# Kernel optimization log

Measured on AMD Instinct MI355X. Metric: run time of the kernel, lower is better.

## Reference

```python
import jax, jax.numpy as jnp
import numpy as np

B, T, D = 8, 1024, 1024
H, HS = 16, 64  # num_heads, head_size; H*HS == D


def setup_inputs() -> dict:
    key = jax.random.key(0)
    ks = jax.random.split(key, 5)
    scale = 0.02
    x = jax.random.normal(ks[0], (B, T, D), dtype=jnp.float32)
    Wq = jax.random.normal(ks[1], (H, D, HS), dtype=jnp.float32) * scale
    Wk = jax.random.normal(ks[2], (H, D, HS), dtype=jnp.float32) * scale
    Wv = jax.random.normal(ks[3], (H, D, HS), dtype=jnp.float32) * scale
    Wo = jax.random.normal(ks[4], (D, D), dtype=jnp.float32) * scale
    bo = jnp.zeros((D,), dtype=jnp.float32)
    return {"x": x, "Wq": Wq, "Wk": Wk, "Wv": Wv, "Wo": Wo, "bo": bo}


def reference(x, Wq, Wk, Wv, Wo, bo):
    # Per-head linear projections (bias-free, as in Head): [B,H,T,HS]
    q = jnp.einsum('btd,hds->bhts', x, Wq)
    k = jnp.einsum('btd,hds->bhts', x, Wk)
    v = jnp.einsum('btd,hds->bhts', x, Wv)
    # Scaled scores with causal mask: [B,H,T,T]
    scores = jnp.einsum('bhts,bhus->bhtu', q, k) * (HS ** -0.5)
    causal = jnp.tril(jnp.ones((T, T), dtype=bool))
    scores = jnp.where(causal, scores, jnp.finfo(scores.dtype).min)
    att = jax.nn.softmax(scores, axis=-1)
    # Weighted sum over values, then concat heads: [B,T,H*HS]
    out = jnp.einsum('bhtu,bhus->bhts', att, v)
    out = out.transpose(0, 2, 1, 3).reshape(B, T, H * HS)
    # Output projection (nn.Linear: y = x @ W^T + b)
    return out @ Wo.T + bo
```

## Files before the change

### kernel.cpp

```cpp
#include <hip/hip_runtime.h>
#include <hip/hip_bf16.h>

#define BBATCH 8
#define TSEQ   1024
#define DMODEL 1024
#define NHEAD  16
#define HSZ    64

typedef unsigned short ushort_t;
typedef __attribute__((ext_vector_type(8))) short short8;
typedef __attribute__((ext_vector_type(4))) float float4v;

__device__ __forceinline__ ushort_t f2bf(float f) {
    __hip_bfloat16 h = __float2bfloat16(f);
    return *reinterpret_cast<ushort_t*>(&h);
}
__device__ __forceinline__ ushort_t f2bf_fast(float f) {
    return (ushort_t)((__float_as_uint(f) + 0x8000u) >> 16);
}
__device__ __forceinline__ unsigned int pack_bf2(float lo, float hi) {
    unsigned int a = __float_as_uint(lo) + 0x8000u;
    unsigned int b = __float_as_uint(hi) + 0x8000u;
    return __builtin_amdgcn_perm(b, a, 0x07060302u);
}

__device__ __forceinline__ short8 cvt8(const float* f) {
    union { ushort_t u[8]; short8 v; } r;
    #pragma unroll
    for (int e = 0; e < 8; ++e) r.u[e] = f2bf(f[e]);
    return r.v;
}

__device__ __forceinline__ void async16(const ushort_t* g, ushort_t* l) {
    __builtin_amdgcn_global_load_lds(
        (const __attribute__((address_space(1))) unsigned int*)g,
        (__attribute__((address_space(3))) unsigned int*)l, 16, 0, 0);
}

template<int N> __device__ __forceinline__ void vwait() {
    if constexpr (N == 3)      asm volatile("s_waitcnt vmcnt(3)" ::: "memory");
    else if constexpr (N == 0) asm volatile("s_waitcnt vmcnt(0)" ::: "memory");
}

__global__ __launch_bounds__(256) void cvt_f32_bf16(
    const float* __restrict__ src, ushort_t* __restrict__ dst)
{
    const size_t idx = ((size_t)blockIdx.x * 256 + threadIdx.x) * 16;
    float f[16];
    *(float4*)(f + 0)  = *(const float4*)(src + idx);
    *(float4*)(f + 4)  = *(const float4*)(src + idx + 4);
    *(float4*)(f + 8)  = *(const float4*)(src + idx + 8);
    *(float4*)(f + 12) = *(const float4*)(src + idx + 12);
    uint4 o0 = make_uint4(pack_bf2(f[0], f[1]),   pack_bf2(f[2], f[3]),
                          pack_bf2(f[4], f[5]),   pack_bf2(f[6], f[7]));
    uint4 o1 = make_uint4(pack_bf2(f[8], f[9]),   pack_bf2(f[10], f[11]),
                          pack_bf2(f[12], f[13]), pack_bf2(f[14], f[15]));
    *(uint4*)(dst + idx) = o0;
    *(uint4*)(dst + idx + 8) = o1;
}

__global__ __launch_bounds__(256) void pack_w(
    const float* __restrict__ Wq, const float* __restrict__ Wk,
    const float* __restrict__ Wv, ushort_t* __restrict__ WpT)
{
    __shared__ ushort_t L[64 * 72];
    const int tid = threadIdx.x;
    const int d0 = blockIdx.x * 64;
    const int wh = blockIdx.y;
    const int w = wh >> 4, h = wh & 15;
    const float* W = (w == 0 ? Wq : (w == 1 ? Wk : Wv)) + (size_t)h * DMODEL * HSZ;

    int dr = tid >> 2, sc = (tid & 3) * 16;
    const float4* src = (const float4*)(W + (size_t)(d0 + dr) * HSZ + sc);
    float f[16];
    *(float4*)(f + 0) = src[0]; *(float4*)(f + 4) = src[1];
    *(float4*)(f + 8) = src[2]; *(float4*)(f + 12) = src[3];
    *(short8*)(L + dr * 72 + sc)     = cvt8(f);
    *(short8*)(L + dr * 72 + sc + 8) = cvt8(f + 8);
    __syncthreads();

    int s = tid >> 2, dc = (tid & 3) * 16;
    union { ushort_t u[16]; short8 v[2]; } o;
    #pragma unroll
    for (int j = 0; j < 16; ++j) o.u[j] = L[(dc + j) * 72 + s];
    ushort_t* dst = WpT + (size_t)(w * 1024 + h * 64 + s) * DMODEL + d0 + dc;
    *(short8*)dst = o.v[0];
    *(short8*)(dst + 8) = o.v[1];
}

template<bool STG, int VW>
__device__ __forceinline__ void kstep32(
    const ushort_t* Ab, const ushort_t* Bb,
    ushort_t* An, ushort_t* Bn,
    const ushort_t*& gA, const ushort_t*& gB,
    const int wave,
    const int (&aoff)[4], const int (&boff)[4],
    float4v (&acc)[4][4])
{
    short8 av[4], bv[4];
    #pragma unroll
    for (int a = 0; a < 4; ++a) av[a] = *(const short8*)(Ab + aoff[a]);
    #pragma unroll
    for (int b = 0; b < 4; ++b) bv[b] = *(const short8*)(Bb + boff[b]);
    if (STG) {
        async16(gA,                An + wave * 512);
        async16(gB,                Bn + wave * 512);
        async16(gB + 128 * DMODEL, Bn + 4096 + wave * 512);
        gA += 32; gB += 32;
    }
    __builtin_amdgcn_s_setprio(1);
    #pragma unroll
    for (int a = 0; a < 4; ++a)
        #pragma unroll
        for (int b = 0; b < 4; ++b)
            acc[a][b] = __builtin_amdgcn_mfma_f32_16x16x32_bf16(
                av[a], bv[b], acc[a][b], 0, 0, 0);
    __builtin_amdgcn_s_setprio(0);
    vwait<VW>();
    __builtin_amdgcn_s_barrier();
}

__global__ __launch_bounds__(512, 4) void qkv_gemm(
    const ushort_t* __restrict__ Xb, const ushort_t* __restrict__ WpT,
    ushort_t* __restrict__ Qb, ushort_t* __restrict__ Kb, ushort_t* __restrict__ Vt)
{
    __shared__ ushort_t Ab[3][128 * 32];
    __shared__ ushort_t Bb[3][256 * 32];

    const int tid = threadIdx.x;
    const int wave = tid >> 6, lane = tid & 63;
    const int q = lane >> 4, cc = lane & 15;
    const int wm = wave >> 2, wn = wave & 3;

    const int bid = blockIdx.x;
    const int xcd = bid & 7;
    const bool isV = (bid >= 512);
    int ta, tb;
    if (!isV) {
        int lo = bid >> 3;
        ta = lo >> 2;
        tb = xcd * 4 + (lo & 3);
    } else {
        int lo = (bid - 512) >> 3;
        ta = xcd * 8 + (lo & 7);
        tb = lo >> 3;
    }
    const ushort_t* pA = isV ? Xb  + (size_t)ta * 128 * DMODEL
                             : WpT + (size_t)ta * 128 * DMODEL;
    const ushort_t* pB = isV ? WpT + (size_t)(2048 + tb * 256) * DMODEL
                             : Xb  + (size_t)tb * 256 * DMODEL;

    const int srow = lane >> 2;
    const int chx = (lane & 3) ^ ((lane >> 3) & 3);
    const ushort_t* gA = pA + (size_t)(wave * 16 + srow) * DMODEL + chx * 8;
    const ushort_t* gB = pB + (size_t)(wave * 16 + srow) * DMODEL + chx * 8;

    int aoff[4], boff[4];
    const int cswz = (q ^ ((cc >> 1) & 3)) * 8;
    #pragma unroll
    for (int f = 0; f < 4; ++f) {
        aoff[f] = (wm * 64 + f * 16 + cc) * 32 + cswz;
        boff[f] = (wn * 64 + f * 16 + cc) * 32 + cswz;
    }

    float4v acc[4][4];
    #pragma unroll
    for (int a = 0; a < 4; ++a)
        #pragma unroll
        for (int b = 0; b < 4; ++b) acc[a][b] = (float4v){0.f, 0.f, 0.f, 0.f};

    async16(gA,                Ab[0] + wave * 512);
    async16(gB,                Bb[0] + wave * 512);
    async16(gB + 128 * DMODEL, Bb[0] + 4096 + wave * 512);
    gA += 32; gB += 32;
    async16(gA,                Ab[1] + wave * 512);
    async16(gB,                Bb[1] + wave * 512);
    async16(gB + 128 * DMODEL, Bb[1] + 4096 + wave * 512);
    gA += 32; gB += 32;
    vwait<3>();
    __builtin_amdgcn_s_barrier();

    #pragma unroll 1
    for (int it = 0; it < 10; ++it) {
        kstep32<true, 3>(Ab[0], Bb[0], Ab[2], Bb[2], gA, gB, wave, aoff, boff, acc);
        kstep32<true, 3>(Ab[1], Bb[1], Ab[0], Bb[0], gA, gB, wave, aoff, boff, acc);
        kstep32<true, 3>(Ab[2], Bb[2], Ab[1], Bb[1], gA, gB, wave, aoff, boff, acc);
    }
    kstep32<false, 0>(Ab[0], Bb[0], Ab[2], Bb[2], gA, gB, wave, aoff, boff, acc);
    kstep32<false, -1>(Ab[1], Bb[1], Ab[0], Bb[0], gA, gB, wave, aoff, boff, acc);

    if (!isV) {
        ushort_t* Out = (ta < 8) ? Qb : Kb;
        const float osc = (ta < 8) ? 0.18033688011112042f : 1.0f;
        const int h = ((ta * 128 + wm * 64) >> 6) & 15;
        #pragma unroll
        for (int b = 0; b < 4; ++b) {
            int mc = tb * 256 + wn * 64 + b * 16 + cc;
            int bb = mc >> 10, t = mc & 1023;
            size_t rb = (((size_t)(bb * NHEAD + h)) * TSEQ + t) * HSZ;
            #pragma unroll
            for (int a = 0; a < 4; ++a) {
                int s0 = a * 16 + q * 4;
                uint2 pk = make_uint2(
                    pack_bf2(acc[a][b][0] * osc, acc[a][b][1] * osc),
                    pack_bf2(acc[a][b][2] * osc, acc[a][b][3] * osc));
                *(uint2*)(Out + rb + s0) = pk;
            }
        }
    } else {
        #pragma unroll
        for (int b = 0; b < 4; ++b) {
            int nc = tb * 256 + wn * 64 + b * 16 + cc;
            int h = nc >> 6, s = nc & 63;
            #pragma unroll
            for (int a = 0; a < 4; ++a) {
                int mr = ta * 128 + wm * 64 + a * 16 + q * 4;
                int bb = mr >> 10, t0 = mr & 1023;
                size_t addr = (((size_t)(bb * NHEAD + h)) * HSZ + s) * TSEQ + t0;
                uint2 pk = make_uint2(pack_bf2(acc[a][b][0], acc[a][b][1]),
                                      pack_bf2(acc[a][b][2], acc[a][b][3]));
                *(uint2*)(Vt + addr) = pk;
            }
        }
    }
}

__global__ __launch_bounds__(256) void attn(
    const ushort_t* __restrict__ Qb, const ushort_t* __restrict__ Kb,
    const ushort_t* __restrict__ Vt, ushort_t* __restrict__ Ob)
{
    __shared__ ushort_t Ks[2][64 * 64];
    __shared__ ushort_t VTs[2][64 * 64];
    __shared__ ushort_t Ps[4][32 * 72];
    const int tid = threadIdx.x;
    const int wave = tid >> 6, lane = tid & 63;
    const int q = lane >> 4, cc = lane & 15;
    const int bid = blockIdx.x;
    const int qt = 7 - (bid >> 7);
    const int bh = bid & 127;
    const size_t base = (size_t)bh * TSEQ * HSZ;
    const int J = 2 * qt + 2;

    const ushort_t* kg[2]; const ushort_t* vg[2]; int dmo[2];
    #pragma unroll
    for (int i = 0; i < 2; ++i) {
        int rr = wave * 16 + i * 8 + (lane >> 3);
        int ch = (lane & 7) ^ (rr & 7);
        kg[i] = Kb + base + (size_t)rr * HSZ + ch * 8;
        vg[i] = Vt + base + (size_t)rr * TSEQ + ch * 8;
        dmo[i] = (wave * 16 + i * 8) * 64;
    }

    short8 qf[2][2];
    #pragma unroll
    for (int tt = 0; tt < 2; ++tt) {
        const ushort_t* qp = Qb + base +
            (size_t)(qt * 128 + wave * 32 + tt * 16 + cc) * HSZ + q * 8;
        qf[tt][0] = *(const short8*)qp;
        qf[tt][1] = *(const short8*)(qp + 32);
    }

    int koff[4][2], poff[2][2];
    #pragma unroll
    for (int ut = 0; ut < 4; ++ut)
        #pragma unroll
        for (int kt = 0; kt < 2; ++kt)
            koff[ut][kt] = (ut * 16 + cc) * 64 + (((kt * 4 + q) ^ (cc & 7)) * 8);
    #pragma unroll
    for (int tt = 0; tt < 2; ++tt)
        #pragma unroll
        for (int kt = 0; kt < 2; ++kt)
            poff[tt][kt] = (tt * 16 + cc) * 72 + kt * 32 + q * 8;

    float4v oacc[2][4];
    #pragma unroll
    for (int tt = 0; tt < 2; ++tt)
        #pragma unroll
        for (int st = 0; st < 4; ++st) oacc[tt][st] = (float4v){0.f, 0.f, 0.f, 0.f};
    float lsum[2] = {0.f, 0.f};

    #pragma unroll
    for (int i = 0; i < 2; ++i) {
        async16(kg[i], &Ks[0][dmo[i]]);
        async16(vg[i], &VTs[0][dmo[i]]);
    }
    __syncthreads();

    for (int jt = 0; jt < J; ++jt) {
        const ushort_t* Kc = Ks[jt & 1];
        const ushort_t* Vc = VTs[jt & 1];
        if (jt + 1 < J) {
            int nb = (jt + 1) & 1;
            #pragma unroll
            for (int i = 0; i < 2; ++i) {
                async16(kg[i] + (size_t)(jt + 1) * 64 * HSZ, &Ks[nb][dmo[i]]);
                async16(vg[i] + (jt + 1) * 64, &VTs[nb][dmo[i]]);
            }
        }

        float4v sc[4][2];
        #pragma unroll
        for (int ut = 0; ut < 4; ++ut)
            #pragma unroll
            for (int tt = 0; tt < 2; ++tt) sc[ut][tt] = (float4v){0.f, 0.f, 0.f, 0.f};
        #pragma unroll
        for (int kt = 0; kt < 2; ++kt) {
            short8 kf[4];
            #pragma unroll
            for (int ut = 0; ut < 4; ++ut) kf[ut] = *(const short8*)(Kc + koff[ut][kt]);
            #pragma unroll
            for (int ut = 0; ut < 4; ++ut) {
                sc[ut][0] = __builtin_amdgcn_mfma_f32_16x16x32_bf16(
                    kf[ut], qf[0][kt], sc[ut][0], 0, 0, 0);
                sc[ut][1] = __builtin_amdgcn_mfma_f32_16x16x32_bf16(
                    kf[ut], qf[1][kt], sc[ut][1], 0, 0, 0);
            }
        }

        if ((jt >> 1) == qt) {
            #pragma unroll
            for (int tt = 0; tt < 2; ++tt) {
                const int tg = qt * 128 + wave * 32 + tt * 16 + cc;
                #pragma unroll
                for (int ut = 0; ut < 4; ++ut) {
                    float pv[4]; float ps = 0.f;
                    #pragma unroll
                    for (int rr = 0; rr < 4; ++rr) {
                        float p = exp2f(sc[ut][tt][rr]);
                        if ((jt * 64 + ut * 16 + q * 4 + rr) > tg) p = 0.f;
                        pv[rr] = p; ps += p;
                    }
                    lsum[tt] += ps;
                    *(uint2*)&Ps[wave][(tt * 16 + cc) * 72 + ut * 16 + q * 4] =
                        make_uint2(pack_bf2(pv[0], pv[1]), pack_bf2(pv[2], pv[3]));
                }
            }
        } else {
            #pragma unroll
            for (int tt = 0; tt < 2; ++tt) {
                #pragma unroll
                for (int ut = 0; ut < 4; ++ut) {
                    float pv[4]; float ps = 0.f;
                    #pragma unroll
                    for (int rr = 0; rr < 4; ++rr) {
                        float p = exp2f(sc[ut][tt][rr]);
                        pv[rr] = p; ps += p;
                    }
                    lsum[tt] += ps;
                    *(uint2*)&Ps[wave][(tt * 16 + cc) * 72 + ut * 16 + q * 4] =
                        make_uint2(pack_bf2(pv[0], pv[1]), pack_bf2(pv[2], pv[3]));
                }
            }
        }

        #pragma unroll
        for (int kt = 0; kt < 2; ++kt) {
            short8 pa0 = *(const short8*)&Ps[wave][poff[0][kt]];
            short8 pa1 = *(const short8*)&Ps[wave][poff[1][kt]];
            #pragma unroll
            for (int st = 0; st < 4; ++st) {
                short8 vf = *(const short8*)(Vc + koff[st][kt]);
                oacc[0][st] = __builtin_amdgcn_mfma_f32_16x16x32_bf16(
                    pa0, vf, oacc[0][st], 0, 0, 0);
                oacc[1][st] = __builtin_amdgcn_mfma_f32_16x16x32_bf16(
                    pa1, vf, oacc[1][st], 0, 0, 0);
            }
        }
        __syncthreads();
    }

    float inv[2];
    #pragma unroll
    for (int tt = 0; tt < 2; ++tt) {
        float l = lsum[tt];
        l += __shfl_xor(l, 16);
        l += __shfl_xor(l, 32);
        inv[tt] = 1.f / l;
    }
    const int b = bh >> 4, h = bh & 15;
    #pragma unroll
    for (int tt = 0; tt < 2; ++tt)
        #pragma unroll
        for (int rr = 0; rr < 4; ++rr) {
            float iv = __shfl(inv[tt], q * 4 + rr);
            int t = qt * 128 + wave * 32 + tt * 16 + q * 4 + rr;
            size_t rb = ((size_t)b * TSEQ + t) * DMODEL + h * HSZ;
            #pragma unroll
            for (int st = 0; st < 4; ++st)
                Ob[rb + st * 16 + cc] = f2bf_fast(oacc[tt][st][rr] * iv);
        }
}

__global__ __launch_bounds__(256) void oproj_gemm(
    const ushort_t* __restrict__ Obuf, const ushort_t* __restrict__ Wob,
    const float* __restrict__ bo, float* __restrict__ out)
{
    __shared__ ushort_t As[128 * 64];
    __shared__ ushort_t Bs[128 * 64];
    const int tid = threadIdx.x;
    const int wave = tid >> 6, lane = tid & 63;
    const int q = lane >> 4, cc = lane & 15;
    const int bid = blockIdx.x;
    const int xcd = bid & 7, local = bid >> 3;
    const int n0 = (local >> 3) * 128;
    const int m0 = (xcd * 8 + (local & 7)) * 128;
    const int wm = wave >> 1, wn = wave & 1;

    const ushort_t* ag[4]; const ushort_t* bg[4]; int lo_[4];
    #pragma unroll
    for (int i = 0; i < 4; ++i) {
        int row = wave * 32 + i * 8 + (lane >> 3);
        int ch = (lane & 7) ^ (row & 7);
        ag[i] = Obuf + (size_t)(m0 + row) * DMODEL + ch * 8;
        bg[i] = Wob + (size_t)(n0 + row) * DMODEL + ch * 8;
        lo_[i] = (wave * 32 + i * 8) * 64;
    }
    int aoff[4][2], boff[4][2];
    #pragma unroll
    for (int mt = 0; mt < 4; ++mt) {
        int row = wm * 64 + mt * 16 + cc;
        #pragma unroll
        for (int kt = 0; kt < 2; ++kt)
            aoff[mt][kt] = row * 64 + (((kt * 4 + q) ^ (row & 7)) * 8);
    }
    #pragma unroll
    for (int nt = 0; nt < 4; ++nt) {
        int row = wn * 64 + nt * 16 + cc;
        #pragma unroll
        for (int kt = 0; kt < 2; ++kt)
            boff[nt][kt] = row * 64 + (((kt * 4 + q) ^ (row & 7)) * 8);
    }

    float4v acc[4][4];
    #pragma unroll
    for (int a = 0; a < 4; ++a)
        #pragma unroll
        for (int b = 0; b < 4; ++b) acc[a][b] = (float4v){0.f, 0.f, 0.f, 0.f};

    for (int j = 0; j < 16; ++j) {
        #pragma unroll
        for (int i = 0; i < 4; ++i) {
            async16(ag[i], As + lo_[i]);
            async16(bg[i], Bs + lo_[i]);
            ag[i] += 64; bg[i] += 64;
        }
        __syncthreads();

        short8 av[4][2], bv[4][2];
        #pragma unroll
        for (int mt = 0; mt < 4; ++mt) {
            av[mt][0] = *(const short8*)(As + aoff[mt][0]);
            av[mt][1] = *(const short8*)(As + aoff[mt][1]);
        }
        #pragma unroll
        for (int nt = 0; nt < 4; ++nt) {
            bv[nt][0] = *(const short8*)(Bs + boff[nt][0]);
            bv[nt][1] = *(const short8*)(Bs + boff[nt][1]);
        }
        #pragma unroll
        for (int kt = 0; kt < 2; ++kt)
            #pragma unroll
            for (int mt = 0; mt < 4; ++mt)
                #pragma unroll
                for (int nt = 0; nt < 4; ++nt)
                    acc[mt][nt] = __builtin_amdgcn_mfma_f32_16x16x32_bf16(
                        av[mt][kt], bv[nt][kt], acc[mt][nt], 0, 0, 0);
        __syncthreads();
    }

    #pragma unroll
    for (int nt = 0; nt < 4; ++nt) {
        int n = n0 + wn * 64 + nt * 16 + cc;
        float bias = bo[n];
        #pragma unroll
        for (int mt = 0; mt < 4; ++mt)
            #pragma unroll
            for (int rr = 0; rr < 4; ++rr) {
                int m = m0 + wm * 64 + mt * 16 + q * 4 + rr;
                out[(size_t)m * DMODEL + n] = acc[mt][nt][rr] + bias;
            }
    }
}

extern "C" void kernel_launch(void* const* d_in, const int* in_sizes, int n_in,
                              void* d_out, int out_size, void* d_ws, size_t ws_size,
                              hipStream_t stream)
{
    const float* x  = (const float*)d_in[0];
    const float* Wq = (const float*)d_in[1];
    const float* Wk = (const float*)d_in[2];
    const float* Wv = (const float*)d_in[3];
    const float* Wo = (const float*)d_in[4];
    const float* bo = (const float*)d_in[5];
    float* out = (float*)d_out;

    const size_t SEG = (size_t)8 * 1024 * 1024;
    ushort_t* Qb  = (ushort_t*)d_ws;
    ushort_t* Kb  = Qb + SEG;
    ushort_t* Vtb = Kb + SEG;
    ushort_t* WpT = Vtb + SEG;
    ushort_t* Ob  = WpT;
    ushort_t* Xb  = (ushort_t*)d_out;
    ushort_t* Wob = Qb;

    cvt_f32_bf16<<<dim3(2048),    256, 0, stream>>>(x, Xb);
    pack_w      <<<dim3(16, 48),  256, 0, stream>>>(Wq, Wk, Wv, WpT);
    qkv_gemm    <<<dim3(768),     512, 0, stream>>>(Xb, WpT, Qb, Kb, Vtb);
    attn        <<<dim3(1024),    256, 0, stream>>>(Qb, Kb, Vtb, Ob);
    cvt_f32_bf16<<<dim3(256),     256, 0, stream>>>(Wo, Wob);
    oproj_gemm  <<<dim3(512),     256, 0, stream>>>(Ob, Wob, bo, out);
}
```

Measured before the change: 226.1 us.

## Merge prep kernels, pipeline oproj GEMM, raise MFMA priority in attention

After: 237.6 us. 5.1% more time.

```diff
diff --git a/kernel.cpp b/kernel.cpp
--- a/kernel.cpp
+++ b/kernel.cpp
@@ -42,10 +42,9 @@
     else if constexpr (N == 0) asm volatile("s_waitcnt vmcnt(0)" ::: "memory");
 }
 
-__global__ __launch_bounds__(256) void cvt_f32_bf16(
-    const float* __restrict__ src, ushort_t* __restrict__ dst)
-{
-    const size_t idx = ((size_t)blockIdx.x * 256 + threadIdx.x) * 16;
+__device__ __forceinline__ void cvt16(const float* __restrict__ src,
+                                      ushort_t* __restrict__ dst, size_t idx)
+{
     float f[16];
     *(float4*)(f + 0)  = *(const float4*)(src + idx);
     *(float4*)(f + 4)  = *(const float4*)(src + idx + 4);
@@ -59,14 +58,28 @@
     *(uint4*)(dst + idx + 8) = o1;
 }
 
-__global__ __launch_bounds__(256) void pack_w(
+__global__ __launch_bounds__(256) void cvt_f32_bf16(
+    const float* __restrict__ src, ushort_t* __restrict__ dst)
+{
+    cvt16(src, dst, ((size_t)blockIdx.x * 256 + threadIdx.x) * 16);
+}
+
+__global__ __launch_bounds__(256) void prep(
+    const float* __restrict__ x,
     const float* __restrict__ Wq, const float* __restrict__ Wk,
-    const float* __restrict__ Wv, ushort_t* __restrict__ WpT)
+    const float* __restrict__ Wv,
+    ushort_t* __restrict__ Xb, ushort_t* __restrict__ WpT)
 {
     __shared__ ushort_t L[64 * 72];
+    const int bid = blockIdx.x;
     const int tid = threadIdx.x;
-    const int d0 = blockIdx.x * 64;
-    const int wh = blockIdx.y;
+    if (bid < 2048) {
+        cvt16(x, Xb, ((size_t)bid * 256 + tid) * 16);
+        return;
+    }
+    const int idx = bid - 2048;
+    const int d0 = (idx & 15) * 64;
+    const int wh = idx >> 4;
     const int w = wh >> 4, h = wh & 15;
     const float* W = (w == 0 ? Wq : (w == 1 ? Wk : Wv)) + (size_t)h * DMODEL * HSZ;
 
@@ -118,6 +131,31 @@
     __builtin_amdgcn_s_setprio(0);
     vwait<VW>();
     __builtin_amdgcn_s_barrier();
+}
+
+__device__ __forceinline__ void gemm_loop32(
+    ushort_t (*Ab)[128 * 32], ushort_t (*Bb)[256 * 32],
+    const ushort_t*& gA, const ushort_t*& gB, const int wave,
+    const int (&aoff)[4], const int (&boff)[4], float4v (&acc)[4][4])
+{
+    #pragma unroll 1
+    for (int it = 0; it < 10; ++it) {
+        kstep32<true, 3>(Ab[0], Bb[0], Ab[2], Bb[2], gA, gB, wave, aoff, boff, acc);
+        kstep32<true, 3>(Ab[1], Bb[1], Ab[0], Bb[0], gA, gB, wave, aoff, boff, acc);
+        kstep32<true, 3>(Ab[2], Bb[2], Ab[1], Bb[1], gA, gB, wave, aoff, boff, acc);
+    }
+    kstep32<false, 0>(Ab[0], Bb[0], Ab[2], Bb[2], gA, gB, wave, aoff, boff, acc);
+    kstep32<false, -1>(Ab[1], Bb[1], Ab[0], Bb[0], gA, gB, wave, aoff, boff, acc);
+}
+
+__device__ __forceinline__ void stage_full(
+    ushort_t* Abuf, ushort_t* Bbuf,
+    const ushort_t*& gA, const ushort_t*& gB, const int wave)
+{
+    async16(gA,                Abuf + wave * 512);
+    async16(gB,                Bbuf + wave * 512);
+    async16(gB + 128 * DMODEL, Bbuf + 4096 + wave * 512);
+    gA += 32; gB += 32;
 }
 
 __global__ __launch_bounds__(512, 4) void qkv_gemm(
@@ -169,25 +207,12 @@
         #pragma unroll
         for (int b = 0; b < 4; ++b) acc[a][b] = (float4v){0.f, 0.f, 0.f, 0.f};
 
-    async16(gA,                Ab[0] + wave * 512);
-    async16(gB,                Bb[0] + wave * 512);
-    async16(gB + 128 * DMODEL, Bb[0] + 4096 + wave * 512);
-    gA += 32; gB += 32;
-    async16(gA,                Ab[1] + wave * 512);
-    async16(gB,                Bb[1] + wave * 512);
-    async16(gB + 128 * DMODEL, Bb[1] + 4096 + wave * 512);
-    gA += 32; gB += 32;
+    stage_full(Ab[0], Bb[0], gA, gB, wave);
+    stage_full(Ab[1], Bb[1], gA, gB, wave);
     vwait<3>();
     __builtin_amdgcn_s_barrier();
 
-    #pragma unroll 1
-    for (int it = 0; it < 10; ++it) {
-        kstep32<true, 3>(Ab[0], Bb[0], Ab[2], Bb[2], gA, gB, wave, aoff, boff, acc);
-        kstep32<true, 3>(Ab[1], Bb[1], Ab[0], Bb[0], gA, gB, wave, aoff, boff, acc);
-        kstep32<true, 3>(Ab[2], Bb[2], Ab[1], Bb[1], gA, gB, wave, aoff, boff, acc);
-    }
-    kstep32<false, 0>(Ab[0], Bb[0], Ab[2], Bb[2], gA, gB, wave, aoff, boff, acc);
-    kstep32<false, -1>(Ab[1], Bb[1], Ab[0], Bb[0], gA, gB, wave, aoff, boff, acc);
+    gemm_loop32(Ab, Bb, gA, gB, wave, aoff, boff, acc);
 
     if (!isV) {
         ushort_t* Out = (ta < 8) ? Qb : Kb;
@@ -308,6 +333,7 @@
             short8 kf[4];
             #pragma unroll
             for (int ut = 0; ut < 4; ++ut) kf[ut] = *(const short8*)(Kc + koff[ut][kt]);
+            __builtin_amdgcn_s_setprio(1);
             #pragma unroll
             for (int ut = 0; ut < 4; ++ut) {
                 sc[ut][0] = __builtin_amdgcn_mfma_f32_16x16x32_bf16(
@@ -315,6 +341,7 @@
                 sc[ut][1] = __builtin_amdgcn_mfma_f32_16x16x32_bf16(
                     kf[ut], qf[1][kt], sc[ut][1], 0, 0, 0);
             }
+            __builtin_amdgcn_s_setprio(0);
         }
 
         if ((jt >> 1) == qt) {
@@ -357,6 +384,7 @@
         for (int kt = 0; kt < 2; ++kt) {
             short8 pa0 = *(const short8*)&Ps[wave][poff[0][kt]];
             short8 pa1 = *(const short8*)&Ps[wave][poff[1][kt]];
+            __builtin_amdgcn_s_setprio(1);
             #pragma unroll
             for (int st = 0; st < 4; ++st) {
                 short8 vf = *(const short8*)(Vc + koff[st][kt]);
@@ -365,6 +393,7 @@
                 oacc[1][st] = __builtin_amdgcn_mfma_f32_16x16x32_bf16(
                     pa1, vf, oacc[1][st], 0, 0, 0);
             }
+            __builtin_amdgcn_s_setprio(0);
         }
         __syncthreads();
     }
@@ -391,44 +420,37 @@
         }
 }
 
-__global__ __launch_bounds__(256) void oproj_gemm(
+__global__ __launch_bounds__(512, 4) void oproj_gemm(
     const ushort_t* __restrict__ Obuf, const ushort_t* __restrict__ Wob,
     const float* __restrict__ bo, float* __restrict__ out)
 {
-    __shared__ ushort_t As[128 * 64];
-    __shared__ ushort_t Bs[128 * 64];
+    __shared__ ushort_t Ab[3][128 * 32];
+    __shared__ ushort_t Bb[3][256 * 32];
+
     const int tid = threadIdx.x;
     const int wave = tid >> 6, lane = tid & 63;
     const int q = lane >> 4, cc = lane & 15;
+    const int wm = wave >> 2, wn = wave & 3;
+
     const int bid = blockIdx.x;
-    const int xcd = bid & 7, local = bid >> 3;
-    const int n0 = (local >> 3) * 128;
-    const int m0 = (xcd * 8 + (local & 7)) * 128;
-    const int wm = wave >> 1, wn = wave & 1;
-
-    const ushort_t* ag[4]; const ushort_t* bg[4]; int lo_[4];
-    #pragma unroll
-    for (int i = 0; i < 4; ++i) {
-        int row = wave * 32 + i * 8 + (lane >> 3);
-        int ch = (lane & 7) ^ (row & 7);
-        ag[i] = Obuf + (size_t)(m0 + row) * DMODEL + ch * 8;
-        bg[i] = Wob + (size_t)(n0 + row) * DMODEL + ch * 8;
-        lo_[i] = (wave * 32 + i * 8) * 64;
-    }
-    int aoff[4][2], boff[4][2];
-    #pragma unroll
-    for (int mt = 0; mt < 4; ++mt) {
-        int row = wm * 64 + mt * 16 + cc;
-        #pragma unroll
-        for (int kt = 0; kt < 2; ++kt)
-            aoff[mt][kt] = row * 64 + (((kt * 4 + q) ^ (row & 7)) * 8);
-    }
-    #pragma unroll
-    for (int nt = 0; nt < 4; ++nt) {
-        int row = wn * 64 + nt * 16 + cc;
-        #pragma unroll
-        for (int kt = 0; kt < 2; ++kt)
-            boff[nt][kt] = row * 64 + (((kt * 4 + q) ^ (row & 7)) * 8);
+    const int xcd = bid & 7, lo = bid >> 3;
+    const int ta = xcd * 8 + (lo & 7);
+    const int tb = lo >> 3;
+
+    const ushort_t* pA = Obuf + (size_t)ta * 128 * DMODEL;
+    const ushort_t* pB = Wob  + (size_t)tb * 256 * DMODEL;
+
+    const int srow = lane >> 2;
+    const int chx = (lane & 3) ^ ((lane >> 3) & 3);
+    const ushort_t* gA = pA + (size_t)(wave * 16 + srow) * DMODEL + chx * 8;
+    const ushort_t* gB = pB + (size_t)(wave * 16 + srow) * DMODEL + chx * 8;
+
+    int aoff[4], boff[4];
+    const int cswz = (q ^ ((cc >> 1) & 3)) * 8;
+    #pragma unroll
+    for (int f = 0; f < 4; ++f) {
+        aoff[f] = (wm * 64 + f * 16 + cc) * 32 + cswz;
+        boff[f] = (wn * 64 + f * 16 + cc) * 32 + cswz;
     }
 
     float4v acc[4][4];
@@ -437,48 +459,25 @@
         #pragma unroll
         for (int b = 0; b < 4; ++b) acc[a][b] = (float4v){0.f, 0.f, 0.f, 0.f};
 
-    for (int j = 0; j < 16; ++j) {
-        #pragma unroll
-        for (int i = 0; i < 4; ++i) {
-            async16(ag[i], As + lo_[i]);
-            async16(bg[i], Bs + lo_[i]);
-            ag[i] += 64; bg[i] += 64;
-        }
-        __syncthreads();
-
-        short8 av[4][2], bv[4][2];
-        #pragma unroll
-        for (int mt = 0; mt < 4; ++mt) {
-            av[mt][0] = *(const short8*)(As + aoff[mt][0]);
-            av[mt][1] = *(const short8*)(As + aoff[mt][1]);
-        }
-        #pragma unroll
-        for (int nt = 0; nt < 4; ++nt) {
-            bv[nt][0] = *(const short8*)(Bs + boff[nt][0]);
-            bv[nt][1] = *(const short8*)(Bs + boff[nt][1]);
-        }
-        #pragma unroll
-        for (int kt = 0; kt < 2; ++kt)
-            #pragma unroll
-            for (int mt = 0; mt < 4; ++mt)
-                #pragma unroll
-                for (int nt = 0; nt < 4; ++nt)
-                    acc[mt][nt] = __builtin_amdgcn_mfma_f32_16x16x32_bf16(
-                        av[mt][kt], bv[nt][kt], acc[mt][nt], 0, 0, 0);
-        __syncthreads();
-    }
-
-    #pragma unroll
-    for (int nt = 0; nt < 4; ++nt) {
-        int n = n0 + wn * 64 + nt * 16 + cc;
+    stage_full(Ab[0], Bb[0], gA, gB, wave);
+    stage_full(Ab[1], Bb[1], gA, gB, wave);
+    vwait<3>();
+    __builtin_amdgcn_s_barrier();
+
+    gemm_loop32(Ab, Bb, gA, gB, wave, aoff, boff, acc);
+
+    #pragma unroll
+    for (int b = 0; b < 4; ++b) {
+        int n = tb * 256 + wn * 64 + b * 16 + cc;
         float bias = bo[n];
         #pragma unroll
-        for (int mt = 0; mt < 4; ++mt)
+        for (int a = 0; a < 4; ++a) {
             #pragma unroll
             for (int rr = 0; rr < 4; ++rr) {
-                int m = m0 + wm * 64 + mt * 16 + q * 4 + rr;
-                out[(size_t)m * DMODEL + n] = acc[mt][nt][rr] + bias;
-            }
+                int m = ta * 128 + wm * 64 + a * 16 + q * 4 + rr;
+                out[(size_t)m * DMODEL + n] = acc[a][b][rr] + bias;
+            }
+        }
     }
 }
 
@@ -503,10 +502,9 @@
     ushort_t* Xb  = (ushort_t*)d_out;
     ushort_t* Wob = Qb;
 
-    cvt_f32_bf16<<<dim3(2048),    256, 0, stream>>>(x, Xb);
-    pack_w      <<<dim3(16, 48),  256, 0, stream>>>(Wq, Wk, Wv, WpT);
+    prep        <<<dim3(2816),    256, 0, stream>>>(x, Wq, Wk, Wv, Xb, WpT);
     qkv_gemm    <<<dim3(768),     512, 0, stream>>>(Xb, WpT, Qb, Kb, Vtb);
     attn        <<<dim3(1024),    256, 0, stream>>>(Qb, Kb, Vtb, Ob);
     cvt_f32_bf16<<<dim3(256),     256, 0, stream>>>(Wo, Wob);
-    oproj_gemm  <<<dim3(512),     256, 0, stream>>>(Ob, Wob, bo, out);
-}
+    oproj_gemm  <<<dim3(256),     512, 0, stream>>>(Ob, Wob, bo, out);
+}
```
